# Kernel tuning notes

Hardware: AMD Instinct MI355X
Metric: run time of the kernel (lower is better)

Reference implementation:

```python
import jax, jax.numpy as jnp
import numpy as np

B, S, D, H, BLK = 2, 2048, 1024, 16, 128
DH = D // H
NB = S // BLK
EPS = 1e-5
NEG = -1e9


def _make_layout():
    i = np.arange(NB)[:, None]
    j = np.arange(NB)[None, :]
    # causal: local block diagonal + previous block + global first block column
    lay = ((j == i) | (j == i - 1) | (j == 0)) & (j <= i)
    return jnp.asarray(np.broadcast_to(lay, (H, NB, NB)).astype(np.int32))


def setup_inputs() -> dict:
    key = jax.random.key(0)
    ks = jax.random.split(key, 8)
    sd = 1.0 / np.sqrt(D)
    inp = {
        "x": jax.random.normal(ks[0], (B, S, D), jnp.float32),
        "ln1_g": jnp.ones((D,), jnp.float32),
        "ln1_b": jnp.zeros((D,), jnp.float32),
        "Wq": jax.random.normal(ks[1], (D, D), jnp.float32) * sd,
        "bq": jnp.zeros((D,), jnp.float32),
        "Wk": jax.random.normal(ks[2], (D, D), jnp.float32) * sd,
        "bk": jnp.zeros((D,), jnp.float32),
        "Wv": jax.random.normal(ks[3], (D, D), jnp.float32) * sd,
        "bv": jnp.zeros((D,), jnp.float32),
        "Wo": jax.random.normal(ks[4], (D, D), jnp.float32) * sd,
        "bo": jnp.zeros((D,), jnp.float32),
        "ln2_g": jnp.ones((D,), jnp.float32),
        "ln2_b": jnp.zeros((D,), jnp.float32),
        "W1": jax.random.normal(ks[5], (D, 4 * D), jnp.float32) * sd,
        "b1": jnp.zeros((4 * D,), jnp.float32),
        "W2": jax.random.normal(ks[6], (4 * D, D), jnp.float32) * (1.0 / np.sqrt(4 * D)),
        "b2": jnp.zeros((D,), jnp.float32),
        "layout": _make_layout(),
    }
    return inp


def _ln(x, g, b):
    m = jnp.mean(x, -1, keepdims=True)
    v = jnp.var(x, -1, keepdims=True)
    return (x - m) * jax.lax.rsqrt(v + EPS) * g + b


def reference(x, ln1_g, ln1_b, Wq, bq, Wk, bk, Wv, bv, Wo, bo,
              ln2_g, ln2_b, W1, b1, W2, b2, layout):
    # ---- pre-norm block-sparse multi-head attention + residual ----
    h = _ln(x, ln1_g, ln1_b)
    q = (h @ Wq + bq).reshape(B, S, H, DH).transpose(0, 2, 1, 3)
    k = (h @ Wk + bk).reshape(B, S, H, DH).transpose(0, 2, 1, 3)
    v = (h @ Wv + bv).reshape(B, S, H, DH).transpose(0, 2, 1, 3)

    # expand block layout [H,NB,NB] -> token mask [H,S,S], intersect with causal
    blk_mask = jnp.repeat(jnp.repeat(layout > 0, BLK, axis=1), BLK, axis=2)
    causal = jnp.tril(jnp.ones((S, S), bool))
    mask = blk_mask & causal  # [H,S,S]

    scale = DH ** -0.5
    scores = jnp.einsum("bhqd,bhkd->bhqk", q * scale, k)
    scores = jnp.where(mask[None], scores, NEG)
    att = jax.nn.softmax(scores, axis=-1)
    ctx = jnp.einsum("bhqk,bhkd->bhqd", att, v)
    ctx = ctx.transpose(0, 2, 1, 3).reshape(B, S, D)
    x = x + (ctx @ Wo + bo)

    # ---- pre-norm MLP (GeLU) + residual ----
    h2 = _ln(x, ln2_g, ln2_b)
    ff = jax.nn.gelu(h2 @ W1 + b1, approximate=False) @ W2 + b2
    return x + ff
```

## Files before the change

### kernel.cpp

```cpp
#include <hip/hip_runtime.h>

typedef unsigned short ushort;
typedef unsigned int uint;
typedef __attribute__((ext_vector_type(8))) short short8;
typedef __attribute__((ext_vector_type(4))) float floatx4;

#define DEV __device__ __forceinline__

DEV ushort f2bf(float f) {
    uint u = __float_as_uint(f);
    u += 0x7fffu + ((u >> 16) & 1u);
    return (ushort)(u >> 16);
}

DEV void load_lds16(const void* g, const void* l) {
    __builtin_amdgcn_global_load_lds(
        (const __attribute__((address_space(1))) void*)g,
        (__attribute__((address_space(3))) void*)l, 16, 0, 0);
}

template<int ROWS>
DEV void stage_tile(const ushort* g, int ldg, ushort* lds, int w, int lane) {
#pragma unroll
    for (int t = 0; t < ROWS / 32; ++t) {
        int row = t * 32 + w * 8 + (lane >> 3);
        int cg  = (lane & 7) ^ (row & 7);
        load_lds16(g + (size_t)row * ldg + cg * 8, lds + (t * 32 + w * 8) * 64);
    }
}

DEV short8 frag_ld(const ushort* lds, int row, int ks, int quad) {
    int slot = (ks * 4 + quad) ^ (row & 7);
    return *(const short8*)(lds + row * 64 + slot * 8);
}

__global__ __launch_bounds__(256) void prep_kernel(
    const float* __restrict__ Wq, const float* __restrict__ Wk,
    const float* __restrict__ Wv, const float* __restrict__ Wo,
    const float* __restrict__ W1, const float* __restrict__ W2,
    const float* __restrict__ bq, const float* __restrict__ bk,
    const float* __restrict__ bv,
    ushort* __restrict__ wqkvT, ushort* __restrict__ woT,
    ushort* __restrict__ w1T, ushort* __restrict__ w2T,
    float* __restrict__ bqkv) {
    __shared__ float t[64][65];
    int bid = blockIdx.x;
    const float* in; ushort* out; int K, N, tx, ty;
    if (bid < 1024) {
        int m = bid >> 8, r = bid & 255;
        in  = m == 0 ? Wq : (m == 1 ? Wk : (m == 2 ? Wv : Wo));
        out = m < 3 ? wqkvT + (size_t)m * 1024 * 1024 : woT;
        K = 1024; N = 1024; tx = r & 15; ty = r >> 4;
    } else if (bid < 2048) {
        int r = bid - 1024; in = W1; out = w1T; K = 1024; N = 4096; tx = r & 63; ty = r >> 6;
    } else {
        int r = bid - 2048; in = W2; out = w2T; K = 4096; N = 1024; tx = r & 15; ty = r >> 4;
    }
    int txx = threadIdx.x & 63, tyy = threadIdx.x >> 6;
    int k0 = ty * 64, n0 = tx * 64;
#pragma unroll
    for (int r2 = tyy; r2 < 64; r2 += 4)
        t[r2][txx] = in[(size_t)(k0 + r2) * N + n0 + txx];
    __syncthreads();
#pragma unroll
    for (int r2 = tyy; r2 < 64; r2 += 4)
        out[(size_t)(n0 + r2) * K + k0 + txx] = f2bf(t[txx][r2]);
    if (bid < 12) {
        int i = bid * 256 + threadIdx.x;
        bqkv[i] = i < 1024 ? bq[i] : (i < 2048 ? bk[i - 1024] : bv[i - 2048]);
    }
}

__global__ __launch_bounds__(256) void ln_kernel(const float* __restrict__ x,
                                                 const float* __restrict__ g,
                                                 const float* __restrict__ bb,
                                                 ushort* __restrict__ out) {
    int row = blockIdx.x, tid = threadIdx.x;
    float4 v = ((const float4*)(x + (size_t)row * 1024))[tid];
    float s = v.x + v.y + v.z + v.w;
    float q = v.x * v.x + v.y * v.y + v.z * v.z + v.w * v.w;
#pragma unroll
    for (int m = 1; m < 64; m <<= 1) {
        s += __shfl_xor(s, m);
        q += __shfl_xor(q, m);
    }
    __shared__ float ss[4], qs[4];
    int w = tid >> 6;
    if ((tid & 63) == 0) { ss[w] = s; qs[w] = q; }
    __syncthreads();
    s = ss[0] + ss[1] + ss[2] + ss[3];
    q = qs[0] + qs[1] + qs[2] + qs[3];
    float mean = s * (1.0f / 1024.0f);
    float var  = q * (1.0f / 1024.0f) - mean * mean;
    float rs   = rsqrtf(var + 1e-5f);
    float4 gv = ((const float4*)g)[tid];
    float4 bv = ((const float4*)bb)[tid];
    ushort o0 = f2bf((v.x - mean) * rs * gv.x + bv.x);
    ushort o1 = f2bf((v.y - mean) * rs * gv.y + bv.y);
    ushort o2 = f2bf((v.z - mean) * rs * gv.z + bv.z);
    ushort o3 = f2bf((v.w - mean) * rs * gv.w + bv.w);
    uint lo = o0 | ((uint)o1 << 16), hi = o2 | ((uint)o3 << 16);
    ((uint2*)(out + (size_t)row * 1024))[tid] = make_uint2(lo, hi);
}

__global__ __launch_bounds__(256) void combine2(const float* __restrict__ p,
                                                const float* __restrict__ res,
                                                const float* __restrict__ bias,
                                                float* __restrict__ out,
                                                int MN, int N) {
    int idx = (blockIdx.x * 256 + threadIdx.x) * 4;
    float4 a = *(const float4*)(p + idx);
    float4 b = *(const float4*)(p + MN + idx);
    float4 r = *(const float4*)(res + idx);
    float4 bi = *(const float4*)(bias + (idx & (N - 1)));
    float4 o;
    o.x = a.x + b.x + r.x + bi.x;
    o.y = a.y + b.y + r.y + bi.y;
    o.z = a.z + b.z + r.z + bi.z;
    o.w = a.w + b.w + r.w + bi.w;
    *(float4*)(out + idx) = o;
}

template<int MODE, int JN>
__global__ __launch_bounds__(256) void gemm128(const ushort* __restrict__ A,
                                               const ushort* __restrict__ Bt,
                                               const float* __restrict__ bias,
                                               const float* __restrict__ res,
                                               void* __restrict__ outp,
                                               int M, int N, int K, int ksplit,
                                               int stx_n, int per_xcd) {
    constexpr int BN = JN * 32;
    __shared__ ushort smemu[128 * 64 + BN * 64];
    ushort* As = smemu;
    ushort* Bs = smemu + 128 * 64;
    int tid = threadIdx.x, w = tid >> 6, lane = tid & 63;
    int quad = lane >> 4, l15 = lane & 15;
    int wm = w >> 1, wn = w & 1;

    int flat = blockIdx.x;
    int xcd = flat & 7, slot = flat >> 3;
    int st = xcd * per_xcd + (slot >> 4);
    int li = slot & 15;
    int bx = (st % stx_n) * 4 + (li & 3);
    int by = (st / stx_n) * 4 + (li >> 2);
    int m0 = by * 128, n0 = bx * BN;
    int sk = blockIdx.y, KS = K / ksplit;

    floatx4 acc[4][JN] = {};
    for (int k0 = sk * KS; k0 < sk * KS + KS; k0 += 64) {
        __syncthreads();
        stage_tile<128>(A + (size_t)m0 * K + k0, K, As, w, lane);
        stage_tile<BN>(Bt + (size_t)n0 * K + k0, K, Bs, w, lane);
        __syncthreads();
#pragma unroll
        for (int ks = 0; ks < 2; ++ks) {
            short8 af[4], bfr[JN];
#pragma unroll
            for (int i = 0; i < 4; ++i) af[i] = frag_ld(As, wm * 64 + i * 16 + l15, ks, quad);
#pragma unroll
            for (int j = 0; j < JN; ++j) bfr[j] = frag_ld(Bs, wn * (JN * 16) + j * 16 + l15, ks, quad);
#pragma unroll
            for (int i = 0; i < 4; ++i)
#pragma unroll
                for (int j = 0; j < JN; ++j)
                    acc[i][j] = __builtin_amdgcn_mfma_f32_16x16x32_bf16(bfr[j], af[i], acc[i][j], 0, 0, 0);
        }
    }

    ushort* Sb = smemu;
    float*  Sf = (float*)smemu;
    int rl  = wm * 16 + l15;
    int rl2 = tid >> 3, c8 = tid & 7;
#pragma unroll
    for (int i = 0; i < 4; ++i) {
        __syncthreads();
        if (MODE >= 2) {
#pragma unroll
            for (int j = 0; j < JN; ++j) {
                int cbase = wn * (JN * 16) + j * 16 + quad * 4;
                float4 wv;
                wv.x = acc[i][j][0]; wv.y = acc[i][j][1];
                wv.z = acc[i][j][2]; wv.w = acc[i][j][3];
                *(float4*)(Sf + rl * 68 + cbase) = wv;
            }
        } else {
#pragma unroll
            for (int j = 0; j < JN; ++j) {
                int cbase = wn * (JN * 16) + j * 16 + quad * 4;
                float4 bv4 = *(const float4*)(bias + n0 + cbase);
                float v0 = acc[i][j][0] + bv4.x, v1 = acc[i][j][1] + bv4.y;
                float v2 = acc[i][j][2] + bv4.z, v3 = acc[i][j][3] + bv4.w;
                if (MODE == 1) {
                    v0 = 0.5f * v0 * (1.0f + erff(v0 * 0.70710678118f));
                    v1 = 0.5f * v1 * (1.0f + erff(v1 * 0.70710678118f));
                    v2 = 0.5f * v2 * (1.0f + erff(v2 * 0.70710678118f));
                    v3 = 0.5f * v3 * (1.0f + erff(v3 * 0.70710678118f));
                }
                uint lo = f2bf(v0) | ((uint)f2bf(v1) << 16);
                uint hi = f2bf(v2) | ((uint)f2bf(v3) << 16);
                *(uint2*)(Sb + rl * 136 + cbase) = make_uint2(lo, hi);
            }
        }
        __syncthreads();
        int grow = m0 + (rl2 >> 4) * 64 + i * 16 + (rl2 & 15);
        if (MODE == 3) {
            int gc = n0 + c8 * 8;
            float4 u0 = *(float4*)(Sf + rl2 * 68 + c8 * 8);
            float4 u1 = *(float4*)(Sf + rl2 * 68 + c8 * 8 + 4);
            float* op = (float*)outp + (size_t)sk * M * N + (size_t)grow * N + gc;
            *(float4*)op = u0;
            *(float4*)(op + 4) = u1;
        } else if (MODE == 2) {
            int gc = n0 + c8 * 8;
            float4 u0 = *(float4*)(Sf + rl2 * 68 + c8 * 8);
            float4 u1 = *(float4*)(Sf + rl2 * 68 + c8 * 8 + 4);
            float4 b0 = *(const float4*)(bias + gc);
            float4 b1 = *(const float4*)(bias + gc + 4);
            const float* rp = res + (size_t)grow * N + gc;
            float4 r0 = *(const float4*)rp;
            float4 r1 = *(const float4*)(rp + 4);
            float4 o0, o1;
            o0.x = u0.x + b0.x + r0.x; o0.y = u0.y + b0.y + r0.y;
            o0.z = u0.z + b0.z + r0.z; o0.w = u0.w + b0.w + r0.w;
            o1.x = u1.x + b1.x + r1.x; o1.y = u1.y + b1.y + r1.y;
            o1.z = u1.z + b1.z + r1.z; o1.w = u1.w + b1.w + r1.w;
            float* op = (float*)outp + (size_t)grow * N + gc;
            *(float4*)op = o0;
            *(float4*)(op + 4) = o1;
        } else {
            short8 d0 = *(short8*)(Sb + rl2 * 136 + c8 * 8);
            short8 d1 = *(short8*)(Sb + rl2 * 136 + c8 * 8 + 64);
            if (MODE == 1) {
                ushort* op = (ushort*)outp + (size_t)grow * N + n0 + c8 * 8;
                *(short8*)op = d0;
                *(short8*)(op + 64) = d1;
            } else {
                int b = grow >> 11, s = grow & 2047;
                int which = n0 >> 10, nbase = n0 & 1023;
                int h0 = nbase >> 6;
                size_t b0a = (size_t)which * 4194304 +
                             (((size_t)(b * 16 + h0)) * 2048 + s) * 64 + c8 * 8;
                size_t b1a = (size_t)which * 4194304 +
                             (((size_t)(b * 16 + h0 + 1)) * 2048 + s) * 64 + c8 * 8;
                *(short8*)((ushort*)outp + b0a) = d0;
                *(short8*)((ushort*)outp + b1a) = d1;
            }
        }
    }
}

__global__ __launch_bounds__(256) void attn_kernel(const ushort* __restrict__ qg,
                                                   const ushort* __restrict__ kg,
                                                   const ushort* __restrict__ vg,
                                                   ushort* __restrict__ ctx) {
    __shared__ ushort Qs[64 * 64];
    __shared__ ushort Ks[128 * 64];
    __shared__ ushort Vs[64 * 136];
    __shared__ ushort Ps[64 * 136];
    int iq2 = blockIdx.x, h = blockIdx.y, b = blockIdx.z;
    int tid = threadIdx.x, w = tid >> 6, lane = tid & 63;
    int quad = lane >> 4, l15 = lane & 15;
    int iq = iq2 >> 1;

    const ushort* qp    = qg + ((size_t)(b * 16 + h) * 2048 + iq2 * 64) * 64;
    const ushort* kbase = kg + (size_t)(b * 16 + h) * 2048 * 64;
    const ushort* vbase = vg + (size_t)(b * 16 + h) * 2048 * 64;

    stage_tile<64>(qp, 64, Qs, w, lane);

    floatx4 o[4] = {};
    float mi[4], li[4];
#pragma unroll
    for (int r = 0; r < 4; ++r) { mi[r] = -1e30f; li[r] = 0.0f; }

    int jbs[3];
    int nj = 0;
    jbs[nj++] = 0;
    if (iq > 1) jbs[nj++] = iq - 1;
    if (iq > 0) jbs[nj++] = iq;

    for (int ji = 0; ji < nj; ++ji) {
        int jb = jbs[ji];
        __syncthreads();
        stage_tile<128>(kbase + (size_t)jb * 128 * 64, 64, Ks, w, lane);
        {
            int dh = tid & 63, sg = tid >> 6;
            const ushort* vp = vbase + (size_t)jb * 128 * 64;
#pragma unroll
            for (int cc = 0; cc < 8; ++cc) {
                int s0 = sg * 32 + cc * 4;
                ushort e0 = vp[(s0 + 0) * 64 + dh];
                ushort e1 = vp[(s0 + 1) * 64 + dh];
                ushort e2 = vp[(s0 + 2) * 64 + dh];
                ushort e3 = vp[(s0 + 3) * 64 + dh];
                uint lo = e0 | ((uint)e1 << 16), hi = e2 | ((uint)e3 << 16);
                *(uint2*)(Vs + dh * 136 + s0) = make_uint2(lo, hi);
            }
        }
        __syncthreads();

        floatx4 sacc[8] = {};
#pragma unroll
        for (int ks = 0; ks < 2; ++ks) {
            short8 af = frag_ld(Qs, w * 16 + l15, ks, quad);
            short8 bf8[8];
#pragma unroll
            for (int nt = 0; nt < 8; ++nt) bf8[nt] = frag_ld(Ks, nt * 16 + l15, ks, quad);
#pragma unroll
            for (int nt = 0; nt < 8; ++nt)
                sacc[nt] = __builtin_amdgcn_mfma_f32_16x16x32_bf16(af, bf8[nt], sacc[nt], 0, 0, 0);
        }

        float rowmax[4] = {-1e30f, -1e30f, -1e30f, -1e30f};
        bool diag = (jb == iq);
        int rowL0 = (iq2 & 1) * 64 + w * 16 + quad * 4;
#pragma unroll
        for (int nt = 0; nt < 8; ++nt) {
#pragma unroll
            for (int r = 0; r < 4; ++r) {
                float xv = sacc[nt][r] * 0.125f;
                if (diag && (nt * 16 + l15 > rowL0 + r)) xv = -1e30f;
                sacc[nt][r] = xv;
                rowmax[r] = fmaxf(rowmax[r], xv);
            }
        }
#pragma unroll
        for (int r = 0; r < 4; ++r)
#pragma unroll
            for (int m = 1; m < 16; m <<= 1)
                rowmax[r] = fmaxf(rowmax[r], __shfl_xor(rowmax[r], m));

        float alpha[4], rsum[4];
#pragma unroll
        for (int r = 0; r < 4; ++r) {
            float mnew = fmaxf(mi[r], rowmax[r]);
            alpha[r] = __expf(mi[r] - mnew);
            mi[r] = mnew;
            rsum[r] = 0.0f;
        }
#pragma unroll
        for (int nt = 0; nt < 8; ++nt) {
#pragma unroll
            for (int r = 0; r < 4; ++r) {
                float p = __expf(sacc[nt][r] - mi[r]);
                rsum[r] += p;
                Ps[(w * 16 + quad * 4 + r) * 136 + nt * 16 + l15] = f2bf(p);
            }
        }
#pragma unroll
        for (int r = 0; r < 4; ++r) {
#pragma unroll
            for (int m = 1; m < 16; m <<= 1) rsum[r] += __shfl_xor(rsum[r], m);
            li[r] = li[r] * alpha[r] + rsum[r];
        }
#pragma unroll
        for (int nt = 0; nt < 4; ++nt)
#pragma unroll
            for (int r = 0; r < 4; ++r) o[nt][r] *= alpha[r];

#pragma unroll
        for (int ks2 = 0; ks2 < 4; ++ks2) {
            short8 ap = *(const short8*)(Ps + (w * 16 + l15) * 136 + ks2 * 32 + quad * 8);
            short8 bv4[4];
#pragma unroll
            for (int nt = 0; nt < 4; ++nt)
                bv4[nt] = *(const short8*)(Vs + (nt * 16 + l15) * 136 + ks2 * 32 + quad * 8);
#pragma unroll
            for (int nt = 0; nt < 4; ++nt)
                o[nt] = __builtin_amdgcn_mfma_f32_16x16x32_bf16(ap, bv4[nt], o[nt], 0, 0, 0);
        }
    }
#pragma unroll
    for (int nt = 0; nt < 4; ++nt) {
#pragma unroll
        for (int r = 0; r < 4; ++r) {
            int srow = iq2 * 64 + w * 16 + quad * 4 + r;
            float val = o[nt][r] / li[r];
            ctx[((size_t)b * 2048 + srow) * 1024 + h * 64 + nt * 16 + l15] = f2bf(val);
        }
    }
}

extern "C" void kernel_launch(void* const* d_in, const int* in_sizes, int n_in,
                              void* d_out, int out_size, void* d_ws, size_t ws_size,
                              hipStream_t stream) {
    (void)in_sizes; (void)n_in; (void)out_size; (void)ws_size;
    const float* x    = (const float*)d_in[0];
    const float* ln1g = (const float*)d_in[1];
    const float* ln1b = (const float*)d_in[2];
    const float* Wq   = (const float*)d_in[3];
    const float* bq   = (const float*)d_in[4];
    const float* Wk   = (const float*)d_in[5];
    const float* bk   = (const float*)d_in[6];
    const float* Wv   = (const float*)d_in[7];
    const float* bv   = (const float*)d_in[8];
    const float* Wo   = (const float*)d_in[9];
    const float* bo   = (const float*)d_in[10];
    const float* ln2g = (const float*)d_in[11];
    const float* ln2b = (const float*)d_in[12];
    const float* W1   = (const float*)d_in[13];
    const float* b1   = (const float*)d_in[14];
    const float* W2   = (const float*)d_in[15];
    const float* b2   = (const float*)d_in[16];

    char* ws = (char*)d_ws;
    size_t off = 0;
    auto alloc = [&](size_t bytes) {
        char* p = ws + off;
        off += (bytes + 255) & ~(size_t)255;
        return p;
    };
    ushort* wqkvT = (ushort*)alloc((size_t)3072 * 1024 * 2);
    ushort* woT   = (ushort*)alloc((size_t)1024 * 1024 * 2);
    ushort* w1T   = (ushort*)alloc((size_t)1024 * 4096 * 2);
    ushort* w2T   = (ushort*)alloc((size_t)4096 * 1024 * 2);
    float*  bqkv  = (float*)alloc((size_t)3072 * 4);
    ushort* hb    = (ushort*)alloc((size_t)4096 * 1024 * 2);
    ushort* qkvb  = (ushort*)alloc((size_t)3 * 4096 * 1024 * 2);
    ushort* ctx   = (ushort*)alloc((size_t)4096 * 1024 * 2);
    float*  x1    = (float*)alloc((size_t)4096 * 1024 * 4);
    ushort* h2    = (ushort*)alloc((size_t)4096 * 1024 * 2);
    ushort* ub    = (ushort*)alloc((size_t)4096 * 4096 * 2);
    float* w2p = (float*)hb;

    prep_kernel<<<3072, 256, 0, stream>>>(Wq, Wk, Wv, Wo, W1, W2, bq, bk, bv,
                                          wqkvT, woT, w1T, w2T, bqkv);

    ln_kernel<<<4096, 256, 0, stream>>>(x, ln1g, ln1b, hb);

    gemm128<0, 4><<<dim3(768, 1), 256, 0, stream>>>(hb, wqkvT, bqkv, nullptr, qkvb,
                                                    4096, 3072, 1024, 1, 6, 6);

    attn_kernel<<<dim3(32, 16, 2), 256, 0, stream>>>(qkvb, qkvb + 4194304,
                                                     qkvb + 2 * 4194304, ctx);

    gemm128<2, 2><<<dim3(512, 1), 256, 0, stream>>>(ctx, woT, bo, x, x1,
                                                    4096, 1024, 1024, 1, 4, 4);

    ln_kernel<<<4096, 256, 0, stream>>>(x1, ln2g, ln2b, h2);

    gemm128<1, 4><<<dim3(1024, 1), 256, 0, stream>>>(h2, w1T, b1, nullptr, ub,
                                                     4096, 4096, 1024, 1, 8, 8);

    gemm128<3, 2><<<dim3(512, 2), 256, 0, stream>>>(ub, w2T, b2, nullptr, w2p,
                                                    4096, 1024, 4096, 2, 4, 4);
    combine2<<<4096, 256, 0, stream>>>(w2p, x1, b2, (float*)d_out,
                                       4096 * 1024, 1024);
}
```

Measured before the change: 359.7 us.

## Double-buffer GEMM LDS staging, use 128x128 tiles, fuse LN1 into prep

```diff
diff --git a/kernel.cpp b/kernel.cpp
--- a/kernel.cpp
+++ b/kernel.cpp
@@ -42,9 +42,41 @@
     const float* __restrict__ bv,
     ushort* __restrict__ wqkvT, ushort* __restrict__ woT,
     ushort* __restrict__ w1T, ushort* __restrict__ w2T,
-    float* __restrict__ bqkv) {
+    float* __restrict__ bqkv,
+    const float* __restrict__ x, const float* __restrict__ ln1g,
+    const float* __restrict__ ln1b, ushort* __restrict__ hb) {
     __shared__ float t[64][65];
     int bid = blockIdx.x;
+    int tid = threadIdx.x;
+    if (bid >= 3072) {
+        int row = bid - 3072;
+        float4 v = ((const float4*)(x + (size_t)row * 1024))[tid];
+        float s = v.x + v.y + v.z + v.w;
+        float q = v.x * v.x + v.y * v.y + v.z * v.z + v.w * v.w;
+#pragma unroll
+        for (int m = 1; m < 64; m <<= 1) {
+            s += __shfl_xor(s, m);
+            q += __shfl_xor(q, m);
+        }
+        float* ss = &t[0][0];
+        float* qs = &t[1][0];
+        int w = tid >> 6;
+        if ((tid & 63) == 0) { ss[w] = s; qs[w] = q; }
+        __syncthreads();
+        s = ss[0] + ss[1] + ss[2] + ss[3];
+        q = qs[0] + qs[1] + qs[2] + qs[3];
+        float mean = s * (1.0f / 1024.0f);
+        float var  = q * (1.0f / 1024.0f) - mean * mean;
+        float rs   = rsqrtf(var + 1e-5f);
+        float4 gv = ((const float4*)ln1g)[tid];
+        float4 bv4 = ((const float4*)ln1b)[tid];
+        uint lo = f2bf((v.x - mean) * rs * gv.x + bv4.x) |
+                  ((uint)f2bf((v.y - mean) * rs * gv.y + bv4.y) << 16);
+        uint hi = f2bf((v.z - mean) * rs * gv.z + bv4.z) |
+                  ((uint)f2bf((v.w - mean) * rs * gv.w + bv4.w) << 16);
+        ((uint2*)(hb + (size_t)row * 1024))[tid] = make_uint2(lo, hi);
+        return;
+    }
     const float* in; ushort* out; int K, N, tx, ty;
     if (bid < 1024) {
         int m = bid >> 8, r = bid & 255;
@@ -56,7 +88,7 @@
     } else {
         int r = bid - 2048; in = W2; out = w2T; K = 4096; N = 1024; tx = r & 15; ty = r >> 4;
     }
-    int txx = threadIdx.x & 63, tyy = threadIdx.x >> 6;
+    int txx = tid & 63, tyy = tid >> 6;
     int k0 = ty * 64, n0 = tx * 64;
 #pragma unroll
     for (int r2 = tyy; r2 < 64; r2 += 4)
@@ -66,7 +98,7 @@
     for (int r2 = tyy; r2 < 64; r2 += 4)
         out[(size_t)(n0 + r2) * K + k0 + txx] = f2bf(t[txx][r2]);
     if (bid < 12) {
-        int i = bid * 256 + threadIdx.x;
+        int i = bid * 256 + tid;
         bqkv[i] = i < 1024 ? bq[i] : (i < 2048 ? bk[i - 1024] : bv[i - 2048]);
     }
 }
@@ -95,11 +127,10 @@
     float rs   = rsqrtf(var + 1e-5f);
     float4 gv = ((const float4*)g)[tid];
     float4 bv = ((const float4*)bb)[tid];
-    ushort o0 = f2bf((v.x - mean) * rs * gv.x + bv.x);
-    ushort o1 = f2bf((v.y - mean) * rs * gv.y + bv.y);
-    ushort o2 = f2bf((v.z - mean) * rs * gv.z + bv.z);
-    ushort o3 = f2bf((v.w - mean) * rs * gv.w + bv.w);
-    uint lo = o0 | ((uint)o1 << 16), hi = o2 | ((uint)o3 << 16);
+    uint lo = f2bf((v.x - mean) * rs * gv.x + bv.x) |
+              ((uint)f2bf((v.y - mean) * rs * gv.y + bv.y) << 16);
+    uint hi = f2bf((v.z - mean) * rs * gv.z + bv.z) |
+              ((uint)f2bf((v.w - mean) * rs * gv.w + bv.w) << 16);
     ((uint2*)(out + (size_t)row * 1024))[tid] = make_uint2(lo, hi);
 }
 
@@ -121,18 +152,16 @@
     *(float4*)(out + idx) = o;
 }
 
-template<int MODE, int JN>
-__global__ __launch_bounds__(256) void gemm128(const ushort* __restrict__ A,
-                                               const ushort* __restrict__ Bt,
-                                               const float* __restrict__ bias,
-                                               const float* __restrict__ res,
-                                               void* __restrict__ outp,
-                                               int M, int N, int K, int ksplit,
-                                               int stx_n, int per_xcd) {
-    constexpr int BN = JN * 32;
-    __shared__ ushort smemu[128 * 64 + BN * 64];
-    ushort* As = smemu;
-    ushort* Bs = smemu + 128 * 64;
+template<int MODE>
+__global__ __launch_bounds__(256, 2) void gemm_db(const ushort* __restrict__ A,
+                                                  const ushort* __restrict__ Bt,
+                                                  const float* __restrict__ bias,
+                                                  const float* __restrict__ res,
+                                                  void* __restrict__ outp,
+                                                  int M, int N, int K, int ksplit,
+                                                  int stx_n, int per_xcd) {
+    constexpr int BUFE = 256 * 64;
+    __shared__ ushort smem[2 * BUFE];
     int tid = threadIdx.x, w = tid >> 6, lane = tid & 63;
     int quad = lane >> 4, l15 = lane & 15;
     int wm = w >> 1, wn = w & 1;
@@ -143,51 +172,55 @@
     int li = slot & 15;
     int bx = (st % stx_n) * 4 + (li & 3);
     int by = (st / stx_n) * 4 + (li >> 2);
-    int m0 = by * 128, n0 = bx * BN;
+    int m0 = by * 128, n0 = bx * 128;
     int sk = blockIdx.y, KS = K / ksplit;
-
-    floatx4 acc[4][JN] = {};
-    for (int k0 = sk * KS; k0 < sk * KS + KS; k0 += 64) {
+    int kbeg = sk * KS, kend = kbeg + KS;
+
+    const ushort* Ab = A + (size_t)m0 * K;
+    const ushort* Bb = Bt + (size_t)n0 * K;
+
+    stage_tile<128>(Ab + kbeg, K, smem, w, lane);
+    stage_tile<128>(Bb + kbeg, K, smem + 128 * 64, w, lane);
+
+    floatx4 acc[4][4] = {};
+    int cur = 0;
+    for (int k0 = kbeg; k0 < kend; k0 += 64) {
         __syncthreads();
-        stage_tile<128>(A + (size_t)m0 * K + k0, K, As, w, lane);
-        stage_tile<BN>(Bt + (size_t)n0 * K + k0, K, Bs, w, lane);
-        __syncthreads();
+        if (k0 + 64 < kend) {
+            ushort* nb = smem + (cur ^ 1) * BUFE;
+            stage_tile<128>(Ab + k0 + 64, K, nb, w, lane);
+            stage_tile<128>(Bb + k0 + 64, K, nb + 128 * 64, w, lane);
+        }
+        const ushort* Asc = smem + cur * BUFE;
+        const ushort* Bsc = Asc + 128 * 64;
 #pragma unroll
         for (int ks = 0; ks < 2; ++ks) {
-            short8 af[4], bfr[JN];
-#pragma unroll
-            for (int i = 0; i < 4; ++i) af[i] = frag_ld(As, wm * 64 + i * 16 + l15, ks, quad);
-#pragma unroll
-            for (int j = 0; j < JN; ++j) bfr[j] = frag_ld(Bs, wn * (JN * 16) + j * 16 + l15, ks, quad);
+            short8 af[4], bfr[4];
+#pragma unroll
+            for (int i = 0; i < 4; ++i) af[i] = frag_ld(Asc, wm * 64 + i * 16 + l15, ks, quad);
+#pragma unroll
+            for (int j = 0; j < 4; ++j) bfr[j] = frag_ld(Bsc, wn * 64 + j * 16 + l15, ks, quad);
 #pragma unroll
             for (int i = 0; i < 4; ++i)
 #pragma unroll
-                for (int j = 0; j < JN; ++j)
+                for (int j = 0; j < 4; ++j)
                     acc[i][j] = __builtin_amdgcn_mfma_f32_16x16x32_bf16(bfr[j], af[i], acc[i][j], 0, 0, 0);
         }
-    }
-
-    ushort* Sb = smemu;
-    float*  Sf = (float*)smemu;
+        cur ^= 1;
+    }
+
+    ushort* Sb = smem;
+    float*  Sf = (float*)smem;
     int rl  = wm * 16 + l15;
     int rl2 = tid >> 3, c8 = tid & 7;
-#pragma unroll
-    for (int i = 0; i < 4; ++i) {
-        __syncthreads();
-        if (MODE >= 2) {
-#pragma unroll
-            for (int j = 0; j < JN; ++j) {
-                int cbase = wn * (JN * 16) + j * 16 + quad * 4;
-                float4 wv;
-                wv.x = acc[i][j][0]; wv.y = acc[i][j][1];
-                wv.z = acc[i][j][2]; wv.w = acc[i][j][3];
-                *(float4*)(Sf + rl * 68 + cbase) = wv;
-            }
-        } else {
-#pragma unroll
-            for (int j = 0; j < JN; ++j) {
-                int cbase = wn * (JN * 16) + j * 16 + quad * 4;
-                float4 bv4 = *(const float4*)(bias + n0 + cbase);
+    if (MODE <= 1) {
+#pragma unroll
+        for (int i = 0; i < 4; ++i) {
+            __syncthreads();
+#pragma unroll
+            for (int j = 0; j < 4; ++j) {
+                int col = wn * 64 + j * 16 + quad * 4;
+                float4 bv4 = *(const float4*)(bias + n0 + col);
                 float v0 = acc[i][j][0] + bv4.x, v1 = acc[i][j][1] + bv4.y;
                 float v2 = acc[i][j][2] + bv4.z, v3 = acc[i][j][3] + bv4.w;
                 if (MODE == 1) {
@@ -198,38 +231,12 @@
                 }
                 uint lo = f2bf(v0) | ((uint)f2bf(v1) << 16);
                 uint hi = f2bf(v2) | ((uint)f2bf(v3) << 16);
-                *(uint2*)(Sb + rl * 136 + cbase) = make_uint2(lo, hi);
-            }
-        }
-        __syncthreads();
-        int grow = m0 + (rl2 >> 4) * 64 + i * 16 + (rl2 & 15);
-        if (MODE == 3) {
-            int gc = n0 + c8 * 8;
-            float4 u0 = *(float4*)(Sf + rl2 * 68 + c8 * 8);
-            float4 u1 = *(float4*)(Sf + rl2 * 68 + c8 * 8 + 4);
-            float* op = (float*)outp + (size_t)sk * M * N + (size_t)grow * N + gc;
-            *(float4*)op = u0;
-            *(float4*)(op + 4) = u1;
-        } else if (MODE == 2) {
-            int gc = n0 + c8 * 8;
-            float4 u0 = *(float4*)(Sf + rl2 * 68 + c8 * 8);
-            float4 u1 = *(float4*)(Sf + rl2 * 68 + c8 * 8 + 4);
-            float4 b0 = *(const float4*)(bias + gc);
-            float4 b1 = *(const float4*)(bias + gc + 4);
-            const float* rp = res + (size_t)grow * N + gc;
-            float4 r0 = *(const float4*)rp;
-            float4 r1 = *(const float4*)(rp + 4);
-            float4 o0, o1;
-            o0.x = u0.x + b0.x + r0.x; o0.y = u0.y + b0.y + r0.y;
-            o0.z = u0.z + b0.z + r0.z; o0.w = u0.w + b0.w + r0.w;
-            o1.x = u1.x + b1.x + r1.x; o1.y = u1.y + b1.y + r1.y;
-            o1.z = u1.z + b1.z + r1.z; o1.w = u1.w + b1.w + r1.w;
-            float* op = (float*)outp + (size_t)grow * N + gc;
-            *(float4*)op = o0;
-            *(float4*)(op + 4) = o1;
-        } else {
+                *(uint2*)(Sb + rl * 136 + col) = make_uint2(lo, hi);
+            }
+            __syncthreads();
+            int grow = m0 + (rl2 >> 4) * 64 + i * 16 + (rl2 & 15);
             short8 d0 = *(short8*)(Sb + rl2 * 136 + c8 * 8);
-            short8 d1 = *(short8*)(Sb + rl2 * 136 + c8 * 8 + 64);
+            short8 d1 = *(short8*)(Sb + rl2 * 136 + 64 + c8 * 8);
             if (MODE == 1) {
                 ushort* op = (ushort*)outp + (size_t)grow * N + n0 + c8 * 8;
                 *(short8*)op = d0;
@@ -238,12 +245,53 @@
                 int b = grow >> 11, s = grow & 2047;
                 int which = n0 >> 10, nbase = n0 & 1023;
                 int h0 = nbase >> 6;
-                size_t b0a = (size_t)which * 4194304 +
-                             (((size_t)(b * 16 + h0)) * 2048 + s) * 64 + c8 * 8;
-                size_t b1a = (size_t)which * 4194304 +
-                             (((size_t)(b * 16 + h0 + 1)) * 2048 + s) * 64 + c8 * 8;
-                *(short8*)((ushort*)outp + b0a) = d0;
-                *(short8*)((ushort*)outp + b1a) = d1;
+                size_t a0 = (size_t)which * 4194304 +
+                            (((size_t)(b * 16 + h0)) * 2048 + s) * 64 + c8 * 8;
+                size_t a1 = (size_t)which * 4194304 +
+                            (((size_t)(b * 16 + h0 + 1)) * 2048 + s) * 64 + c8 * 8;
+                *(short8*)((ushort*)outp + a0) = d0;
+                *(short8*)((ushort*)outp + a1) = d1;
+            }
+        }
+    } else {
+#pragma unroll
+        for (int i = 0; i < 4; ++i) {
+#pragma unroll
+            for (int hh = 0; hh < 2; ++hh) {
+                __syncthreads();
+                if (wn == hh) {
+#pragma unroll
+                    for (int j = 0; j < 4; ++j) {
+                        float4 wv;
+                        wv.x = acc[i][j][0]; wv.y = acc[i][j][1];
+                        wv.z = acc[i][j][2]; wv.w = acc[i][j][3];
+                        *(float4*)(Sf + rl * 68 + j * 16 + quad * 4) = wv;
+                    }
+                }
+                __syncthreads();
+                int grow = m0 + (rl2 >> 4) * 64 + i * 16 + (rl2 & 15);
+                int gc = n0 + hh * 64 + c8 * 8;
+                float4 u0 = *(float4*)(Sf + rl2 * 68 + c8 * 8);
+                float4 u1 = *(float4*)(Sf + rl2 * 68 + c8 * 8 + 4);
+                if (MODE == 3) {
+                    float* op = (float*)outp + (size_t)sk * M * N + (size_t)grow * N + gc;
+                    *(float4*)op = u0;
+                    *(float4*)(op + 4) = u1;
+                } else {
+                    float4 b0 = *(const float4*)(bias + gc);
+                    float4 b1 = *(const float4*)(bias + gc + 4);
+                    const float* rp = res + (size_t)grow * N + gc;
+                    float4 r0 = *(const float4*)rp;
+                    float4 r1 = *(const float4*)(rp + 4);
+                    float4 o0, o1;
+                    o0.x = u0.x + b0.x + r0.x; o0.y = u0.y + b0.y + r0.y;
+                    o0.z = u0.z + b0.z + r0.z; o0.w = u0.w + b0.w + r0.w;
+                    o1.x = u1.x + b1.x + r1.x; o1.y = u1.y + b1.y + r1.y;
+                    o1.z = u1.z + b1.z + r1.z; o1.w = u1.w + b1.w + r1.w;
+                    float* op = (float*)outp + (size_t)grow * N + gc;
+                    *(float4*)op = o0;
+                    *(float4*)(op + 4) = o1;
+                }
             }
         }
     }
@@ -423,27 +471,26 @@
     ushort* ub    = (ushort*)alloc((size_t)4096 * 4096 * 2);
     float* w2p = (float*)hb;
 
-    prep_kernel<<<3072, 256, 0, stream>>>(Wq, Wk, Wv, Wo, W1, W2, bq, bk, bv,
-                                          wqkvT, woT, w1T, w2T, bqkv);
-
-    ln_kernel<<<4096, 256, 0, stream>>>(x, ln1g, ln1b, hb);
-
-    gemm128<0, 4><<<dim3(768, 1), 256, 0, stream>>>(hb, wqkvT, bqkv, nullptr, qkvb,
-                                                    4096, 3072, 1024, 1, 6, 6);
+    prep_kernel<<<7168, 256, 0, stream>>>(Wq, Wk, Wv, Wo, W1, W2, bq, bk, bv,
+                                          wqkvT, woT, w1T, w2T, bqkv,
+                                          x, ln1g, ln1b, hb);
+
+    gemm_db<0><<<dim3(768, 1), 256, 0, stream>>>(hb, wqkvT, bqkv, nullptr, qkvb,
+                                                 4096, 3072, 1024, 1, 6, 6);
 
     attn_kernel<<<dim3(32, 16, 2), 256, 0, stream>>>(qkvb, qkvb + 4194304,
                                                      qkvb + 2 * 4194304, ctx);
 
-    gemm128<2, 2><<<dim3(512, 1), 256, 0, stream>>>(ctx, woT, bo, x, x1,
-                                                    4096, 1024, 1024, 1, 4, 4);
+    gemm_db<2><<<dim3(256, 1), 256, 0, stream>>>(ctx, woT, bo, x, x1,
+                                                 4096, 1024, 1024, 1, 2, 2);
 
     ln_kernel<<<4096, 256, 0, stream>>>(x1, ln2g, ln2b, h2);
 
-    gemm128<1, 4><<<dim3(1024, 1), 256, 0, stream>>>(h2, w1T, b1, nullptr, ub,
-                                                     4096, 4096, 1024, 1, 8, 8);
-
-    gemm128<3, 2><<<dim3(512, 2), 256, 0, stream>>>(ub, w2T, b2, nullptr, w2p,
-                                                    4096, 1024, 4096, 2, 4, 4);
+    gemm_db<1><<<dim3(1024, 1), 256, 0, stream>>>(h2, w1T, b1, nullptr, ub,
+                                                  4096, 4096, 1024, 1, 8, 8);
+
+    gemm_db<3><<<dim3(256, 2), 256, 0, stream>>>(ub, w2T, b2, nullptr, w2p,
+                                                 4096, 1024, 4096, 2, 2, 2);
     combine2<<<4096, 256, 0, stream>>>(w2p, x1, b2, (float*)d_out,
                                        4096 * 1024, 1024);
 }
```

Measured after the change: 320.3 us. -11.0%, faster.
